# Performance work log

Hardware: AMD Instinct MI355X
Metric: run time of the kernel (lower is better)

The kernel has to match this reference:

```python
import jax, jax.numpy as jnp
import numpy as np

THRESHOLD = 10.0

def _sig(x):
    # sigmoid((x - 0.5) * threshold)
    return jax.nn.sigmoid((x - 0.5) * THRESHOLD)

def _sobel1d(x):
    # Conv1d kernel [-1, 0, 1], padding=1, per-channel (weights are diagonal across channels)
    p = jnp.pad(x, ((0, 0), (0, 0), (1, 1)))
    return p[..., 2:] - p[..., :-2]

def _structs(x_sig, direction):
    # x_sig: [B, C, H, W]
    p = jnp.pad(x_sig, ((0, 0), (0, 0), (1, 1), (1, 1)))
    if direction == 'x':
        # sobelx kernel: w[0,0]=-1, w[2,0]=1 -> out[i,j] = t[i+1,j-1] - t[i-1,j-1]
        bound = _sig(jnp.abs(p[..., 2:, :-2] - p[..., :-2, :-2]))
        s = bound.sum(-2)  # [B, C, W]
    else:
        # sobely kernel: w[0,0]=-1, w[0,2]=1 -> out[i,j] = t[i-1,j+1] - t[i-1,j-1]
        bound = _sig(jnp.abs(p[..., :-2, 2:] - p[..., :-2, :-2]))
        s = bound.sum(-1)  # [B, C, H]
    return jnp.abs(_sobel1d(s)).sum(-1) / 4.0  # [B, C]

def setup_inputs() -> dict:
    key = jax.random.key(0)
    k1, k2 = jax.random.split(key)
    B, C, H, W = 16, 4, 512, 512
    inp = jax.random.uniform(k1, (B, C, H, W), dtype=jnp.float32)
    tgt = jax.random.uniform(k2, (B, C, H, W), dtype=jnp.float32)
    weight = jnp.ones((1, C), dtype=jnp.float32)
    return {"input": inp, "target": tgt, "weight": weight}

def reference(input, target, weight):
    input_sigmoid = _sig(input)
    target_sigmoid = _sig(target)
    input_structs_x = _structs(input_sigmoid, 'x') * weight
    input_structs_y = _structs(input_sigmoid, 'y') * weight
    target_structs_x = _structs(target_sigmoid, 'x') * weight
    target_structs_y = _structs(target_sigmoid, 'y') * weight
    loss = (jnp.abs(input_structs_x - target_structs_x)
            + jnp.abs(input_structs_y - target_structs_y)) / 2.0
    return jnp.mean(loss)
```

## Files before the change

### kernel.cpp

```cpp
#include <hip/hip_runtime.h>

#define WW 512
#define HH 512
#define NPLANES 64
#define NCH 4

__device__ __forceinline__ float sigf(float x) {
    float z = (x - 0.5f) * 10.0f;
    float e = __expf(-z);
    return __builtin_amdgcn_rcpf(1.0f + e);
}

__device__ __forceinline__ void load_sig_row(const float* __restrict__ p, float* o) {
    const float4* p4 = reinterpret_cast<const float4*>(p);
    float4 a = p4[0];
    float4 b = p4[1];
    o[0] = sigf(a.x); o[1] = sigf(a.y); o[2] = sigf(a.z); o[3] = sigf(a.w);
    o[4] = sigf(b.x); o[5] = sigf(b.y); o[6] = sigf(b.z); o[7] = sigf(b.w);
}

__global__ __launch_bounds__(256, 4)
void k_stage1(const float* __restrict__ inp, const float* __restrict__ tgt,
              float* __restrict__ colpart, float* __restrict__ rowsum) {
    const int bid    = blockIdx.x;
    const int tensor = bid >> 8;
    const int plane  = (bid >> 2) & 63;
    const int q      = bid & 3;
    const int tid    = threadIdx.x;
    const int wave   = tid >> 6;
    const int lane   = tid & 63;

    const float* __restrict__ base =
        (tensor == 0 ? inp : tgt) + (size_t)plane * (HH * WW);
    const int r0    = q * 128 + wave * 32;
    const int cbase = lane * 8;

    float prev[8], cur[8], nxt[8], cacc[8];
    #pragma unroll
    for (int k = 0; k < 8; ++k) cacc[k] = 0.0f;

    if (r0 == 0) {
        #pragma unroll
        for (int k = 0; k < 8; ++k) prev[k] = 0.0f;
    } else {
        load_sig_row(base + (size_t)(r0 - 1) * WW + cbase, prev);
    }
    load_sig_row(base + (size_t)r0 * WW + cbase, cur);

    float* __restrict__ rs_out = rowsum + ((size_t)tensor * NPLANES + plane) * HH;

    for (int r = r0; r < r0 + 32; ++r) {
        if (r + 1 < HH) {
            load_sig_row(base + (size_t)(r + 1) * WW + cbase, nxt);
        } else {
            #pragma unroll
            for (int k = 0; k < 8; ++k) nxt[k] = 0.0f;
        }

        #pragma unroll
        for (int k = 0; k < 8; ++k)
            cacc[k] += sigf(fabsf(nxt[k] - prev[k]));

        float lv = __shfl_up(cur[7], 1);
        if (lane == 0)  lv = 0.0f;
        float rv = __shfl_down(cur[0], 1);
        if (lane == 63) rv = 0.0f;

        float hp = sigf(fabsf(cur[1] - lv));
        #pragma unroll
        for (int k = 1; k < 7; ++k)
            hp += sigf(fabsf(cur[k + 1] - cur[k - 1]));
        hp += sigf(fabsf(rv - cur[6]));

        #pragma unroll
        for (int off = 32; off >= 1; off >>= 1)
            hp += __shfl_xor(hp, off);
        if (lane == 0) rs_out[r] = hp;

        #pragma unroll
        for (int k = 0; k < 8; ++k) { prev[k] = cur[k]; cur[k] = nxt[k]; }
    }

    __shared__ float cl[4][WW];
    #pragma unroll
    for (int k = 0; k < 8; ++k) cl[wave][cbase + k] = cacc[k];
    __syncthreads();

    float* __restrict__ cp_out =
        colpart + (((size_t)tensor * NPLANES + plane) * 4 + q) * WW;
    for (int c = tid; c < WW; c += 256)
        cp_out[c] = cl[0][c] + cl[1][c] + cl[2][c] + cl[3][c];
}

__device__ __forceinline__ float Sval(const float* s, int j, float s0) {
    if (j < 0 || j >= 512) return 0.0f;
    if (j == 0) return s0;
    return s[j - 1];
}
__device__ __forceinline__ float term(const float* s, int j, float s0) {
    return fabsf(Sval(s, j + 1, s0) - Sval(s, j - 1, s0));
}

__global__ __launch_bounds__(256)
void k_stage2(const float* __restrict__ colpart, const float* __restrict__ rowsum,
              const float* __restrict__ weight, float* __restrict__ plane_loss) {
    __shared__ float cI[WW], cT[WW], rI[WW], rT[WW];
    const int p   = blockIdx.x;
    const int tid = threadIdx.x;

    for (int c = tid; c < WW; c += 256) {
        const float* a = colpart + (((size_t)0 * NPLANES + p) * 4) * WW + c;
        const float* b = colpart + (((size_t)1 * NPLANES + p) * 4) * WW + c;
        cI[c] = a[0] + a[WW] + a[2 * WW] + a[3 * WW];
        cT[c] = b[0] + b[WW] + b[2 * WW] + b[3 * WW];
        rI[c] = rowsum[((size_t)0 * NPLANES + p) * HH + c];
        rT[c] = rowsum[((size_t)1 * NPLANES + p) * HH + c];
    }
    __syncthreads();

    const float s0 = 3.4267396732f;

    float sIx = 0.f, sTx = 0.f, sIy = 0.f, sTy = 0.f;
    for (int j = tid; j < WW; j += 256) {
        sIx += term(cI, j, s0);
        sTx += term(cT, j, s0);
        sIy += term(rI, j, s0);
        sTy += term(rT, j, s0);
    }
    #pragma unroll
    for (int off = 32; off >= 1; off >>= 1) {
        sIx += __shfl_xor(sIx, off);
        sTx += __shfl_xor(sTx, off);
        sIy += __shfl_xor(sIy, off);
        sTy += __shfl_xor(sTy, off);
    }
    __shared__ float red[4][4];
    const int wave = tid >> 6, lane = tid & 63;
    if (lane == 0) {
        red[wave][0] = sIx; red[wave][1] = sTx;
        red[wave][2] = sIy; red[wave][3] = sTy;
    }
    __syncthreads();
    if (tid == 0) {
        float Ix = 0.f, Tx = 0.f, Iy = 0.f, Ty = 0.f;
        for (int w2 = 0; w2 < 4; ++w2) {
            Ix += red[w2][0]; Tx += red[w2][1];
            Iy += red[w2][2]; Ty += red[w2][3];
        }
        Ix *= 0.25f; Tx *= 0.25f; Iy *= 0.25f; Ty *= 0.25f;
        const float wgt = weight[p & (NCH - 1)];
        plane_loss[p] = 0.5f * (fabsf((Ix - Tx) * wgt) + fabsf((Iy - Ty) * wgt));
    }
}

__global__ void k_stage3(const float* __restrict__ plane_loss, float* __restrict__ out) {
    const int lane = threadIdx.x;
    float v = plane_loss[lane];
    #pragma unroll
    for (int off = 32; off >= 1; off >>= 1)
        v += __shfl_xor(v, off);
    if (lane == 0) out[0] = v * (1.0f / 64.0f);
}

extern "C" void kernel_launch(void* const* d_in, const int* in_sizes, int n_in,
                              void* d_out, int out_size, void* d_ws, size_t ws_size,
                              hipStream_t stream) {
    const float* inp = (const float*)d_in[0];
    const float* tgt = (const float*)d_in[1];
    const float* wgt = (const float*)d_in[2];
    float* ws = (float*)d_ws;

    float* colpart = ws;
    float* rowsum  = ws + 262144;
    float* ploss   = ws + 262144 + 65536;

    k_stage1<<<512, 256, 0, stream>>>(inp, tgt, colpart, rowsum);
    k_stage2<<<64, 256, 0, stream>>>(colpart, rowsum, wgt, ploss);
    k_stage3<<<1, 64, 0, stream>>>(ploss, (float*)d_out);
}
```

Before: 163.4 us.

## Split planes into more strips, drop final reduce kernel via atomics, cheaper sigmoid

Stage 1 now splits each plane into eight row strips of sixteen rows per wave instead of four strips of thirty-two. This doubles the block count to raise occupancy on the GPU, and the row loop is fully unrolled. The third reduction kernel is removed: stage 2 atomically adds each plane's scaled loss into the output, which stage 1 zeroes first. The sigmoid is folded into a single FMA feeding exp2. The cost is twice as much halo row reloading, more column partials for stage 2 to sum, and a float atomic-add order that is no longer deterministic.

After: 208.6 us. 27.6% more time.

```diff
diff --git a/kernel.cpp b/kernel.cpp
--- a/kernel.cpp
+++ b/kernel.cpp
@@ -4,10 +4,10 @@
 #define HH 512
 #define NPLANES 64
 #define NCH 4
+#define NSTRIP 8
 
 __device__ __forceinline__ float sigf(float x) {
-    float z = (x - 0.5f) * 10.0f;
-    float e = __expf(-z);
+    float e = __builtin_amdgcn_exp2f(__builtin_fmaf(x, -14.4269504089f, 7.2134752044f));
     return __builtin_amdgcn_rcpf(1.0f + e);
 }
 
@@ -19,20 +19,23 @@
     o[4] = sigf(b.x); o[5] = sigf(b.y); o[6] = sigf(b.z); o[7] = sigf(b.w);
 }
 
-__global__ __launch_bounds__(256, 4)
+__global__ __launch_bounds__(256, 8)
 void k_stage1(const float* __restrict__ inp, const float* __restrict__ tgt,
-              float* __restrict__ colpart, float* __restrict__ rowsum) {
+              float* __restrict__ colpart, float* __restrict__ rowsum,
+              float* __restrict__ out) {
     const int bid    = blockIdx.x;
-    const int tensor = bid >> 8;
-    const int plane  = (bid >> 2) & 63;
-    const int q      = bid & 3;
+    const int tensor = bid >> 9;
+    const int plane  = (bid >> 3) & 63;
+    const int s      = bid & 7;
     const int tid    = threadIdx.x;
     const int wave   = tid >> 6;
     const int lane   = tid & 63;
 
+    if (bid == 0 && tid == 0) out[0] = 0.0f;
+
     const float* __restrict__ base =
         (tensor == 0 ? inp : tgt) + (size_t)plane * (HH * WW);
-    const int r0    = q * 128 + wave * 32;
+    const int r0    = s * 64 + wave * 16;
     const int cbase = lane * 8;
 
     float prev[8], cur[8], nxt[8], cacc[8];
@@ -49,7 +52,9 @@
 
     float* __restrict__ rs_out = rowsum + ((size_t)tensor * NPLANES + plane) * HH;
 
-    for (int r = r0; r < r0 + 32; ++r) {
+    #pragma unroll
+    for (int rr = 0; rr < 16; ++rr) {
+        const int r = r0 + rr;
         if (r + 1 < HH) {
             load_sig_row(base + (size_t)(r + 1) * WW + cbase, nxt);
         } else {
@@ -87,7 +92,7 @@
     __syncthreads();
 
     float* __restrict__ cp_out =
-        colpart + (((size_t)tensor * NPLANES + plane) * 4 + q) * WW;
+        colpart + (((size_t)tensor * NPLANES + plane) * NSTRIP + s) * WW;
     for (int c = tid; c < WW; c += 256)
         cp_out[c] = cl[0][c] + cl[1][c] + cl[2][c] + cl[3][c];
 }
@@ -103,16 +108,19 @@
 
 __global__ __launch_bounds__(256)
 void k_stage2(const float* __restrict__ colpart, const float* __restrict__ rowsum,
-              const float* __restrict__ weight, float* __restrict__ plane_loss) {
+              const float* __restrict__ weight, float* __restrict__ out) {
     __shared__ float cI[WW], cT[WW], rI[WW], rT[WW];
     const int p   = blockIdx.x;
     const int tid = threadIdx.x;
 
     for (int c = tid; c < WW; c += 256) {
-        const float* a = colpart + (((size_t)0 * NPLANES + p) * 4) * WW + c;
-        const float* b = colpart + (((size_t)1 * NPLANES + p) * 4) * WW + c;
-        cI[c] = a[0] + a[WW] + a[2 * WW] + a[3 * WW];
-        cT[c] = b[0] + b[WW] + b[2 * WW] + b[3 * WW];
+        const float* a = colpart + (((size_t)0 * NPLANES + p) * NSTRIP) * WW + c;
+        const float* b = colpart + (((size_t)1 * NPLANES + p) * NSTRIP) * WW + c;
+        float sa = 0.f, sb = 0.f;
+        #pragma unroll
+        for (int i = 0; i < NSTRIP; ++i) { sa += a[i * WW]; sb += b[i * WW]; }
+        cI[c] = sa;
+        cT[c] = sb;
         rI[c] = rowsum[((size_t)0 * NPLANES + p) * HH + c];
         rT[c] = rowsum[((size_t)1 * NPLANES + p) * HH + c];
     }
@@ -149,17 +157,9 @@
         }
         Ix *= 0.25f; Tx *= 0.25f; Iy *= 0.25f; Ty *= 0.25f;
         const float wgt = weight[p & (NCH - 1)];
-        plane_loss[p] = 0.5f * (fabsf((Ix - Tx) * wgt) + fabsf((Iy - Ty) * wgt));
+        float loss = 0.5f * (fabsf((Ix - Tx) * wgt) + fabsf((Iy - Ty) * wgt));
+        atomicAdd(out, loss * (1.0f / NPLANES));
     }
-}
-
-__global__ void k_stage3(const float* __restrict__ plane_loss, float* __restrict__ out) {
-    const int lane = threadIdx.x;
-    float v = plane_loss[lane];
-    #pragma unroll
-    for (int off = 32; off >= 1; off >>= 1)
-        v += __shfl_xor(v, off);
-    if (lane == 0) out[0] = v * (1.0f / 64.0f);
 }
 
 extern "C" void kernel_launch(void* const* d_in, const int* in_sizes, int n_in,
@@ -171,10 +171,8 @@
     float* ws = (float*)d_ws;
 
     float* colpart = ws;
-    float* rowsum  = ws + 262144;
-    float* ploss   = ws + 262144 + 65536;
+    float* rowsum  = ws + 524288;
 
-    k_stage1<<<512, 256, 0, stream>>>(inp, tgt, colpart, rowsum);
-    k_stage2<<<64, 256, 0, stream>>>(colpart, rowsum, wgt, ploss);
-    k_stage3<<<1, 64, 0, stream>>>(ploss, (float*)d_out);
+    k_stage1<<<1024, 256, 0, stream>>>(inp, tgt, colpart, rowsum, (float*)d_out);
+    k_stage2<<<64, 256, 0, stream>>>(colpart, rowsum, wgt, (float*)d_out);
 }
```
